# Performance work log

Hardware: AMD Instinct MI355X
Metric: run time of the kernel (lower is better)

Reference implementation:

```python
import jax, jax.numpy as jnp
import numpy as np

B, S, D, M = 16, 4096, 512, 2048


def setup_inputs() -> dict:
    key = jax.random.key(0)
    ks = jax.random.split(key, 10)
    init = lambda k, shape, fan: (jax.random.normal(k, shape, jnp.float32) / np.sqrt(fan).astype(np.float32))
    return {
        "x": jax.random.normal(ks[0], (B, S, D), jnp.float32),
        "W_qkv": init(ks[1], (D, 3 * D), D),
        "b_qkv": init(ks[2], (3 * D,), D),
        "W1": init(ks[3], (D, M), D),
        "b1": init(ks[4], (M,), D),
        "W2": init(ks[5], (M, M), M),
        "b2": init(ks[6], (M,), M),
        "W3": init(ks[7], (M, 1), M),
        "b3": init(ks[8], (1,), M),
    }


def reference(x, W_qkv, b_qkv, W1, b1, W2, b2, W3, b3):
    # qkv projection: [B,S,3D] -> split into q,k,v [B,S,D]
    qkv = jnp.einsum("bsd,de->bse", x, W_qkv) + b_qkv
    q, k, v = jnp.split(qkv, 3, axis=-1)
    # Only the last query row of causal SDPA is ever used; the last row of a
    # causal mask is fully unmasked, so this is plain attention of q[:, -1]
    # against all keys. scale=1.0 exactly as in the torch call.
    q_last = q[:, -1]                                  # [B, D]
    scores = jnp.einsum("bd,bsd->bs", q_last, k)       # [B, S], scale = 1.0
    attn = jax.nn.softmax(scores, axis=-1)
    sa_last = jnp.einsum("bs,bsd->bd", attn, v)        # [B, D]
    h = x[:, -1] + sa_last
    h = jax.nn.relu(h @ W1 + b1)
    h = jax.nn.relu(h @ W2 + b2)
    out = h @ W3 + b3                                  # [B, 1]
    return (out, q, k)
```

## Files before the change

kernel.cpp:

```cpp
#include <hip/hip_runtime.h>
#include <hip/hip_bf16.h>

#define B_  16
#define S_  4096
#define D_  512
#define M_  2048
#define ROWS (B_ * S_)
#define N3D  (3 * D_)

typedef __attribute__((ext_vector_type(8))) short bf16x8;
typedef __attribute__((ext_vector_type(4))) float f32x4;


__global__ __launch_bounds__(256) void cvt_x_kernel(const float* __restrict__ x,
                                                    __hip_bfloat16* __restrict__ xb) {
    long i = (long)blockIdx.x * 256 + threadIdx.x;
    const float4* x4 = (const float4*)x;
    float4 a = x4[2 * i], b = x4[2 * i + 1];
    union { __hip_bfloat16 h[8]; int4 v; } u;
    u.h[0] = __float2bfloat16(a.x); u.h[1] = __float2bfloat16(a.y);
    u.h[2] = __float2bfloat16(a.z); u.h[3] = __float2bfloat16(a.w);
    u.h[4] = __float2bfloat16(b.x); u.h[5] = __float2bfloat16(b.y);
    u.h[6] = __float2bfloat16(b.z); u.h[7] = __float2bfloat16(b.w);
    ((int4*)xb)[i] = u.v;
}

__global__ __launch_bounds__(256) void cvt_w_kernel(const float* __restrict__ w,
                                                    __hip_bfloat16* __restrict__ wt) {
    int idx = blockIdx.x * 256 + threadIdx.x;
    int n = idx >> 9, k = idx & 511;
    wt[idx] = __float2bfloat16(w[(long)k * N3D + n]);
}

__global__ __launch_bounds__(256) void gemm_qkv_kernel(
    const __hip_bfloat16* __restrict__ Xb,
    const __hip_bfloat16* __restrict__ Wt,
    const float* __restrict__ bias,
    float* __restrict__ qout, float* __restrict__ kout,
    __hip_bfloat16* __restrict__ vout)
{
    __shared__ __hip_bfloat16 As[128][40];
    __shared__ __hip_bfloat16 Bs[128][40];
    const int tid  = threadIdx.x;
    const int m0   = blockIdx.x * 128;
    const int n0   = blockIdx.y * 128;
    const int wave = tid >> 6, lane = tid & 63;
    const int wm   = (wave >> 1) * 64, wn = (wave & 1) * 64;
    const int quad = lane >> 4, l16 = lane & 15;

    const int srow  = tid >> 2;
    const int skcol = (tid & 3) * 8;

    f32x4 acc[4][4] = {};

    for (int k0 = 0; k0 < 512; k0 += 32) {
        int4 a0 = *(const int4*)(Xb + (long)(m0 + srow)      * 512 + k0 + skcol);
        int4 a1 = *(const int4*)(Xb + (long)(m0 + srow + 64) * 512 + k0 + skcol);
        int4 b0 = *(const int4*)(Wt + (long)(n0 + srow)      * 512 + k0 + skcol);
        int4 b1 = *(const int4*)(Wt + (long)(n0 + srow + 64) * 512 + k0 + skcol);
        __syncthreads();
        *(int4*)&As[srow][skcol]      = a0;
        *(int4*)&As[srow + 64][skcol] = a1;
        *(int4*)&Bs[srow][skcol]      = b0;
        *(int4*)&Bs[srow + 64][skcol] = b1;
        __syncthreads();

        bf16x8 af[4], bf[4];
        #pragma unroll
        for (int t = 0; t < 4; t++) {
            af[t] = *(const bf16x8*)&As[wm + t * 16 + l16][quad * 8];
            bf[t] = *(const bf16x8*)&Bs[wn + t * 16 + l16][quad * 8];
        }
        #pragma unroll
        for (int mt = 0; mt < 4; mt++)
            #pragma unroll
            for (int nt = 0; nt < 4; nt++)
                acc[mt][nt] = __builtin_amdgcn_mfma_f32_16x16x32_bf16(
                    af[mt], bf[nt], acc[mt][nt], 0, 0, 0);
    }

    #pragma unroll
    for (int mt = 0; mt < 4; mt++) {
        #pragma unroll
        for (int nt = 0; nt < 4; nt++) {
            int col = n0 + wn + nt * 16 + l16;
            float bcol = bias[col];
            #pragma unroll
            for (int r = 0; r < 4; r++) {
                int row = m0 + wm + mt * 16 + quad * 4 + r;
                float val = acc[mt][nt][r] + bcol;
                if (col < 512)        qout[(long)row * 512 + col]          = val;
                else if (col < 1024)  kout[(long)row * 512 + (col - 512)]  = val;
                else                  vout[(long)row * 512 + (col - 1024)] = __float2bfloat16(val);
            }
        }
    }
}


__global__ __launch_bounds__(256) void scores_kernel(
    const float* __restrict__ q, const float* __restrict__ k, float* __restrict__ sc)
{
    __shared__ float ql[512];
    int b = blockIdx.x, tid = threadIdx.x;
    const float* qrow = q + (long)(b * S_ + S_ - 1) * 512;
    ql[tid]       = qrow[tid];
    ql[tid + 256] = qrow[tid + 256];
    __syncthreads();
    int wave = tid >> 6, lane = tid & 63;
    int s0 = blockIdx.y * 64;
    float4 q1 = *(const float4*)&ql[lane * 8];
    float4 q2 = *(const float4*)&ql[lane * 8 + 4];
    for (int s = s0 + wave; s < s0 + 64; s += 4) {
        const float4* kr = (const float4*)(k + ((long)b * S_ + s) * 512);
        float4 x1 = kr[lane * 2], x2 = kr[lane * 2 + 1];
        float acc = x1.x * q1.x + x1.y * q1.y + x1.z * q1.z + x1.w * q1.w
                  + x2.x * q2.x + x2.y * q2.y + x2.z * q2.z + x2.w * q2.w;
        #pragma unroll
        for (int off = 32; off; off >>= 1) acc += __shfl_xor(acc, off);
        if (lane == 0) sc[(long)b * S_ + s] = acc;
    }
}

__global__ __launch_bounds__(256) void softmax_kernel(const float* __restrict__ sc,
                                                      float* __restrict__ attn)
{
    int b = blockIdx.x, tid = threadIdx.x;
    __shared__ float red[256];
    const float* row = sc + (long)b * S_;
    float mx = -1e30f;
    for (int s = tid; s < S_; s += 256) mx = fmaxf(mx, row[s]);
    red[tid] = mx; __syncthreads();
    for (int o = 128; o; o >>= 1) { if (tid < o) red[tid] = fmaxf(red[tid], red[tid + o]); __syncthreads(); }
    mx = red[0]; __syncthreads();
    float sum = 0.f;
    float* arow = attn + (long)b * S_;
    for (int s = tid; s < S_; s += 256) { float e = __expf(row[s] - mx); arow[s] = e; sum += e; }
    red[tid] = sum; __syncthreads();
    for (int o = 128; o; o >>= 1) { if (tid < o) red[tid] += red[tid + o]; __syncthreads(); }
    float inv = 1.0f / red[0];
    for (int s = tid; s < S_; s += 256) arow[s] *= inv;
}

__global__ __launch_bounds__(256) void h_init_kernel(const float* __restrict__ x,
                                                     float* __restrict__ h) {
    int i = blockIdx.x * 256 + threadIdx.x;
    int b = i >> 9, d = i & 511;
    h[i] = x[(long)(b * S_ + S_ - 1) * 512 + d];
}

__global__ __launch_bounds__(256) void sa_kernel(const __hip_bfloat16* __restrict__ v,
                                                 const float* __restrict__ attn,
                                                 float* __restrict__ h)
{
    int b  = blockIdx.x;
    int d0 = blockIdx.y * 128;
    int s0 = blockIdx.z * 512;
    int tid = threadIdx.x;
    int dt = (tid & 63) * 2;
    int sg = tid >> 6;
    float a0 = 0.f, a1 = 0.f;
    for (int s = s0 + sg; s < s0 + 512; s += 4) {
        float w = attn[(long)b * S_ + s];
        __hip_bfloat162 vv = *(const __hip_bfloat162*)(v + ((long)(b * S_ + s)) * 512 + d0 + dt);
        float2 vf = __bfloat1622float2(vv);
        a0 += w * vf.x; a1 += w * vf.y;
    }
    atomicAdd(&h[b * 512 + d0 + dt],     a0);
    atomicAdd(&h[b * 512 + d0 + dt + 1], a1);
}


__global__ __launch_bounds__(256) void mlp1_kernel(const float* __restrict__ h,
    const float* __restrict__ W1, const float* __restrict__ b1, float* __restrict__ h1)
{
    int b = blockIdx.x;
    int j = blockIdx.y * 256 + threadIdx.x;
    __shared__ float hs[512];
    hs[threadIdx.x]       = h[b * 512 + threadIdx.x];
    hs[threadIdx.x + 256] = h[b * 512 + threadIdx.x + 256];
    __syncthreads();
    float acc = 0.f;
    for (int k2 = 0; k2 < 512; k2++) acc += hs[k2] * W1[(long)k2 * M_ + j];
    acc += b1[j];
    h1[(long)b * M_ + j] = fmaxf(acc, 0.f);
}

__global__ __launch_bounds__(256) void mlp2_kernel(const float* __restrict__ h1,
    const float* __restrict__ W2, const float* __restrict__ b2, float* __restrict__ h2)
{
    int b = blockIdx.x;
    int j = blockIdx.y * 256 + threadIdx.x;
    __shared__ float hs[2048];
    for (int t = threadIdx.x; t < 2048; t += 256) hs[t] = h1[(long)b * M_ + t];
    __syncthreads();
    float acc = 0.f;
    for (int k2 = 0; k2 < 2048; k2++) acc += hs[k2] * W2[(long)k2 * M_ + j];
    acc += b2[j];
    h2[(long)b * M_ + j] = fmaxf(acc, 0.f);
}

__global__ __launch_bounds__(256) void mlp3_kernel(const float* __restrict__ h2,
    const float* __restrict__ W3, const float* __restrict__ b3, float* __restrict__ out)
{
    int b = blockIdx.x, tid = threadIdx.x;
    __shared__ float red[256];
    float acc = 0.f;
    for (int k2 = tid; k2 < 2048; k2 += 256) acc += h2[(long)b * M_ + k2] * W3[k2];
    red[tid] = acc; __syncthreads();
    for (int o = 128; o; o >>= 1) { if (tid < o) red[tid] += red[tid + o]; __syncthreads(); }
    if (tid == 0) out[b] = red[0] + b3[0];
}


extern "C" void kernel_launch(void* const* d_in, const int* in_sizes, int n_in,
                              void* d_out, int out_size, void* d_ws, size_t ws_size,
                              hipStream_t stream)
{
    const float* x    = (const float*)d_in[0];
    const float* Wqkv = (const float*)d_in[1];
    const float* bqkv = (const float*)d_in[2];
    const float* W1   = (const float*)d_in[3];
    const float* b1   = (const float*)d_in[4];
    const float* W2   = (const float*)d_in[5];
    const float* b2   = (const float*)d_in[6];
    const float* W3   = (const float*)d_in[7];
    const float* b3   = (const float*)d_in[8];

    float* out  = (float*)d_out;
    float* qout = out + 16;
    float* kout = qout + (size_t)ROWS * 512;

    char* ws = (char*)d_ws;
    size_t off = 0;
    auto alloc = [&](size_t bytes) -> char* {
        char* p = ws + off; off += (bytes + 255) & ~(size_t)255; return p;
    };
    __hip_bfloat16* Xb = (__hip_bfloat16*)alloc((size_t)ROWS * 512 * 2);
    __hip_bfloat16* Wt = (__hip_bfloat16*)alloc((size_t)N3D * 512 * 2);
    __hip_bfloat16* Vb = (__hip_bfloat16*)alloc((size_t)ROWS * 512 * 2);
    float* sc   = (float*)alloc((size_t)B_ * S_ * 4);
    float* attn = (float*)alloc((size_t)B_ * S_ * 4);
    float* h    = (float*)alloc((size_t)B_ * 512 * 4);
    float* h1   = (float*)alloc((size_t)B_ * M_ * 4);
    float* h2   = (float*)alloc((size_t)B_ * M_ * 4);

    hipLaunchKernelGGL(cvt_x_kernel,   dim3(ROWS * 512 / 8 / 256), dim3(256), 0, stream, x, Xb);
    hipLaunchKernelGGL(cvt_w_kernel,   dim3(N3D * 512 / 256),      dim3(256), 0, stream, Wqkv, Wt);
    hipLaunchKernelGGL(gemm_qkv_kernel, dim3(ROWS / 128, N3D / 128), dim3(256), 0, stream,
                       Xb, Wt, bqkv, qout, kout, Vb);
    hipLaunchKernelGGL(scores_kernel,  dim3(B_, 64), dim3(256), 0, stream, qout, kout, sc);
    hipLaunchKernelGGL(softmax_kernel, dim3(B_),     dim3(256), 0, stream, sc, attn);
    hipLaunchKernelGGL(h_init_kernel,  dim3(B_ * 512 / 256), dim3(256), 0, stream, x, h);
    hipLaunchKernelGGL(sa_kernel,      dim3(B_, 4, 8), dim3(256), 0, stream, Vb, attn, h);
    hipLaunchKernelGGL(mlp1_kernel,    dim3(B_, 8), dim3(256), 0, stream, h, W1, b1, h1);
    hipLaunchKernelGGL(mlp2_kernel,    dim3(B_, 8), dim3(256), 0, stream, h1, W2, b2, h2);
    hipLaunchKernelGGL(mlp3_kernel,    dim3(B_),    dim3(256), 0, stream, h2, W3, b3, out);
}
```

Baseline: 745.0 us.

## Use direct global-to-LDS loads with swizzle in QKV GEMM and retune helper kernels

The QKV GEMM now stages tiles with global_load_lds directly into XOR-swizzled LDS buffers, adds a trailing barrier, and remaps block IDs to group tiles for L2 reuse. The weight-transpose kernel now goes through a shared-memory tile so both its reads and writes are coalesced. The scores kernel gets twice as many blocks. The MLP kernels split the K dimension across waves, which gives more blocks and better parallelism on the small-batch GEMVs. The risk is that the single-buffered direct-to-LDS path with an extra barrier per iteration may stall, and the swizzle and block-index arithmetic must be exactly right for the results to stay correct.

Measured after the change: 728.3 us. -2.3%, faster.

```diff
diff --git a/kernel.cpp b/kernel.cpp
--- a/kernel.cpp
+++ b/kernel.cpp
@@ -27,9 +27,24 @@
 
 __global__ __launch_bounds__(256) void cvt_w_kernel(const float* __restrict__ w,
                                                     __hip_bfloat16* __restrict__ wt) {
-    int idx = blockIdx.x * 256 + threadIdx.x;
-    int n = idx >> 9, k = idx & 511;
-    wt[idx] = __float2bfloat16(w[(long)k * N3D + n]);
+    __shared__ float t[32][33];
+    int n0 = blockIdx.x * 32;
+    int k0 = blockIdx.y * 32;
+    int c = threadIdx.x & 31, r = threadIdx.x >> 5;
+    #pragma unroll
+    for (int i = 0; i < 4; i++)
+        t[r + 8 * i][c] = w[(long)(k0 + r + 8 * i) * N3D + n0 + c];
+    __syncthreads();
+    #pragma unroll
+    for (int i = 0; i < 4; i++)
+        wt[(long)(n0 + r + 8 * i) * 512 + k0 + c] = __float2bfloat16(t[c][r + 8 * i]);
+}
+
+
+__device__ __forceinline__ void gload16(const __hip_bfloat16* g, __hip_bfloat16* l) {
+    __builtin_amdgcn_global_load_lds(
+        (const __attribute__((address_space(1))) unsigned int*)g,
+        (__attribute__((address_space(3))) unsigned int*)l, 16, 0, 0);
 }
 
 __global__ __launch_bounds__(256) void gemm_qkv_kernel(
@@ -39,37 +54,56 @@
     float* __restrict__ qout, float* __restrict__ kout,
     __hip_bfloat16* __restrict__ vout)
 {
-    __shared__ __hip_bfloat16 As[128][40];
-    __shared__ __hip_bfloat16 Bs[128][40];
+    __shared__ __attribute__((aligned(128))) __hip_bfloat16 As[128 * 32];
+    __shared__ __attribute__((aligned(128))) __hip_bfloat16 Bs[128 * 32];
+
     const int tid  = threadIdx.x;
-    const int m0   = blockIdx.x * 128;
-    const int n0   = blockIdx.y * 128;
     const int wave = tid >> 6, lane = tid & 63;
+
+    int bid = blockIdx.x;
+    int swz = (bid & 7) * 768 + (bid >> 3);
+    const int m0 = (swz / 12) * 128;
+    const int n0 = (swz % 12) * 128;
+
     const int wm   = (wave >> 1) * 64, wn = (wave & 1) * 64;
     const int quad = lane >> 4, l16 = lane & 15;
 
-    const int srow  = tid >> 2;
-    const int skcol = (tid & 3) * 8;
+    const int beta0 = wave * 1024 + lane * 16;
+    const int row0  = beta0 >> 6;
+    const int cb0   = (beta0 & 63) ^ (((beta0 >> 7) & 3) << 4);
+
+    const __hip_bfloat16* aSrc0 = Xb + (long)(m0 + row0)      * 512 + (cb0 >> 1);
+    const __hip_bfloat16* aSrc1 = Xb + (long)(m0 + row0 + 64) * 512 + (cb0 >> 1);
+    const __hip_bfloat16* bSrc0 = Wt + (long)(n0 + row0)      * 512 + (cb0 >> 1);
+    const __hip_bfloat16* bSrc1 = Wt + (long)(n0 + row0 + 64) * 512 + (cb0 >> 1);
+    __hip_bfloat16* aDst0 = As + (beta0 >> 1);
+    __hip_bfloat16* aDst1 = As + ((beta0 + 4096) >> 1);
+    __hip_bfloat16* bDst0 = Bs + (beta0 >> 1);
+    __hip_bfloat16* bDst1 = Bs + ((beta0 + 4096) >> 1);
+
+    int aoff[4], boff[4];
+    #pragma unroll
+    for (int t = 0; t < 4; t++) {
+        int ra = wm + t * 16 + l16;
+        aoff[t] = ra * 32 + ((quad ^ ((ra >> 1) & 3)) << 3);
+        int rb = wn + t * 16 + l16;
+        boff[t] = rb * 32 + ((quad ^ ((rb >> 1) & 3)) << 3);
+    }
 
     f32x4 acc[4][4] = {};
 
     for (int k0 = 0; k0 < 512; k0 += 32) {
-        int4 a0 = *(const int4*)(Xb + (long)(m0 + srow)      * 512 + k0 + skcol);
-        int4 a1 = *(const int4*)(Xb + (long)(m0 + srow + 64) * 512 + k0 + skcol);
-        int4 b0 = *(const int4*)(Wt + (long)(n0 + srow)      * 512 + k0 + skcol);
-        int4 b1 = *(const int4*)(Wt + (long)(n0 + srow + 64) * 512 + k0 + skcol);
-        __syncthreads();
-        *(int4*)&As[srow][skcol]      = a0;
-        *(int4*)&As[srow + 64][skcol] = a1;
-        *(int4*)&Bs[srow][skcol]      = b0;
-        *(int4*)&Bs[srow + 64][skcol] = b1;
+        gload16(aSrc0 + k0, aDst0);
+        gload16(aSrc1 + k0, aDst1);
+        gload16(bSrc0 + k0, bDst0);
+        gload16(bSrc1 + k0, bDst1);
         __syncthreads();
 
         bf16x8 af[4], bf[4];
         #pragma unroll
         for (int t = 0; t < 4; t++) {
-            af[t] = *(const bf16x8*)&As[wm + t * 16 + l16][quad * 8];
-            bf[t] = *(const bf16x8*)&Bs[wn + t * 16 + l16][quad * 8];
+            af[t] = *(const bf16x8*)&As[aoff[t]];
+            bf[t] = *(const bf16x8*)&Bs[boff[t]];
         }
         #pragma unroll
         for (int mt = 0; mt < 4; mt++)
@@ -77,6 +111,8 @@
             for (int nt = 0; nt < 4; nt++)
                 acc[mt][nt] = __builtin_amdgcn_mfma_f32_16x16x32_bf16(
                     af[mt], bf[nt], acc[mt][nt], 0, 0, 0);
+
+        __syncthreads();
     }
 
     #pragma unroll
@@ -108,10 +144,10 @@
     ql[tid + 256] = qrow[tid + 256];
     __syncthreads();
     int wave = tid >> 6, lane = tid & 63;
-    int s0 = blockIdx.y * 64;
+    int s0 = blockIdx.y * 32;
     float4 q1 = *(const float4*)&ql[lane * 8];
     float4 q2 = *(const float4*)&ql[lane * 8 + 4];
-    for (int s = s0 + wave; s < s0 + 64; s += 4) {
+    for (int s = s0 + wave; s < s0 + 32; s += 4) {
         const float4* kr = (const float4*)(k + ((long)b * S_ + s) * 512);
         float4 x1 = kr[lane * 2], x2 = kr[lane * 2 + 1];
         float acc = x1.x * q1.x + x1.y * q1.y + x1.z * q1.z + x1.w * q1.w
@@ -174,30 +210,46 @@
 __global__ __launch_bounds__(256) void mlp1_kernel(const float* __restrict__ h,
     const float* __restrict__ W1, const float* __restrict__ b1, float* __restrict__ h1)
 {
-    int b = blockIdx.x;
-    int j = blockIdx.y * 256 + threadIdx.x;
+    int b  = blockIdx.x;
+    int j0 = blockIdx.y * 64;
+    int tid = threadIdx.x;
+    int j = tid & 63, kg = tid >> 6;
     __shared__ float hs[512];
-    hs[threadIdx.x]       = h[b * 512 + threadIdx.x];
-    hs[threadIdx.x + 256] = h[b * 512 + threadIdx.x + 256];
+    __shared__ float red[256];
+    hs[tid]       = h[b * 512 + tid];
+    hs[tid + 256] = h[b * 512 + tid + 256];
     __syncthreads();
+    const float* wp = W1 + (long)(kg * 128) * M_ + j0 + j;
     float acc = 0.f;
-    for (int k2 = 0; k2 < 512; k2++) acc += hs[k2] * W1[(long)k2 * M_ + j];
-    acc += b1[j];
-    h1[(long)b * M_ + j] = fmaxf(acc, 0.f);
+    #pragma unroll 4
+    for (int k2 = 0; k2 < 128; k2++) acc += hs[kg * 128 + k2] * wp[(long)k2 * M_];
+    red[tid] = acc; __syncthreads();
+    if (kg == 0) {
+        float val = red[j] + red[64 + j] + red[128 + j] + red[192 + j] + b1[j0 + j];
+        h1[(long)b * M_ + j0 + j] = fmaxf(val, 0.f);
+    }
 }
 
 __global__ __launch_bounds__(256) void mlp2_kernel(const float* __restrict__ h1,
     const float* __restrict__ W2, const float* __restrict__ b2, float* __restrict__ h2)
 {
-    int b = blockIdx.x;
-    int j = blockIdx.y * 256 + threadIdx.x;
+    int b  = blockIdx.x;
+    int j0 = blockIdx.y * 64;
+    int tid = threadIdx.x;
+    int j = tid & 63, kg = tid >> 6;
     __shared__ float hs[2048];
-    for (int t = threadIdx.x; t < 2048; t += 256) hs[t] = h1[(long)b * M_ + t];
+    __shared__ float red[256];
+    for (int t = tid; t < 2048; t += 256) hs[t] = h1[(long)b * M_ + t];
     __syncthreads();
+    const float* wp = W2 + (long)(kg * 512) * M_ + j0 + j;
     float acc = 0.f;
-    for (int k2 = 0; k2 < 2048; k2++) acc += hs[k2] * W2[(long)k2 * M_ + j];
-    acc += b2[j];
-    h2[(long)b * M_ + j] = fmaxf(acc, 0.f);
+    #pragma unroll 4
+    for (int k2 = 0; k2 < 512; k2++) acc += hs[kg * 512 + k2] * wp[(long)k2 * M_];
+    red[tid] = acc; __syncthreads();
+    if (kg == 0) {
+        float val = red[j] + red[64 + j] + red[128 + j] + red[192 + j] + b2[j0 + j];
+        h2[(long)b * M_ + j0 + j] = fmaxf(val, 0.f);
+    }
 }
 
 __global__ __launch_bounds__(256) void mlp3_kernel(const float* __restrict__ h2,
@@ -246,14 +298,14 @@
     float* h2   = (float*)alloc((size_t)B_ * M_ * 4);
 
     hipLaunchKernelGGL(cvt_x_kernel,   dim3(ROWS * 512 / 8 / 256), dim3(256), 0, stream, x, Xb);
-    hipLaunchKernelGGL(cvt_w_kernel,   dim3(N3D * 512 / 256),      dim3(256), 0, stream, Wqkv, Wt);
-    hipLaunchKernelGGL(gemm_qkv_kernel, dim3(ROWS / 128, N3D / 128), dim3(256), 0, stream,
+    hipLaunchKernelGGL(cvt_w_kernel,   dim3(48, 16),               dim3(256), 0, stream, Wqkv, Wt);
+    hipLaunchKernelGGL(h_init_kernel,  dim3(B_ * 512 / 256), dim3(256), 0, stream, x, h);
+    hipLaunchKernelGGL(gemm_qkv_kernel, dim3(6144), dim3(256), 0, stream,
                        Xb, Wt, bqkv, qout, kout, Vb);
-    hipLaunchKernelGGL(scores_kernel,  dim3(B_, 64), dim3(256), 0, stream, qout, kout, sc);
-    hipLaunchKernelGGL(softmax_kernel, dim3(B_),     dim3(256), 0, stream, sc, attn);
-    hipLaunchKernelGGL(h_init_kernel,  dim3(B_ * 512 / 256), dim3(256), 0, stream, x, h);
+    hipLaunchKernelGGL(scores_kernel,  dim3(B_, 128), dim3(256), 0, stream, qout, kout, sc);
+    hipLaunchKernelGGL(softmax_kernel, dim3(B_),      dim3(256), 0, stream, sc, attn);
     hipLaunchKernelGGL(sa_kernel,      dim3(B_, 4, 8), dim3(256), 0, stream, Vb, attn, h);
-    hipLaunchKernelGGL(mlp1_kernel,    dim3(B_, 8), dim3(256), 0, stream, h, W1, b1, h1);
-    hipLaunchKernelGGL(mlp2_kernel,    dim3(B_, 8), dim3(256), 0, stream, h1, W2, b2, h2);
-    hipLaunchKernelGGL(mlp3_kernel,    dim3(B_),    dim3(256), 0, stream, h2, W3, b3, out);
-}
+    hipLaunchKernelGGL(mlp1_kernel,    dim3(B_, 32), dim3(256), 0, stream, h, W1, b1, h1);
+    hipLaunchKernelGGL(mlp2_kernel,    dim3(B_, 32), dim3(256), 0, stream, h1, W2, b2, h2);
+    hipLaunchKernelGGL(mlp3_kernel,    dim3(B_),     dim3(256), 0, stream, h2, W3, b3, out);
+}
```
